# Performance work log

Hardware: AMD Instinct MI355X
Metric: run time of the kernel (lower is better)

## Reference

```python
import jax, jax.numpy as jnp
import numpy as np

N = 100000      # nodes
IN = 256        # in_feats
H = 256         # h_feats
C = 2           # num_classes
E = 400000      # edges per relation
DST_MAX = [70000, 80000, 75000]  # dst ranges -> guarantees isolated nodes per relation


def _build_rel(rng, dst_max):
    """Build one relation: edges, degree mask, induced subgraph on non-isolated nodes."""
    src = rng.integers(0, N, size=E)
    dst = rng.integers(0, dst_max, size=E)
    deg = np.bincount(dst, minlength=N)
    keep = np.where(deg > 0)[0].astype(np.int32)   # nodes with in_degree > 0 (original order)
    iso = np.where(deg == 0)[0].astype(np.int32)   # isolated nodes (original order)
    inv = np.full(N, -1, dtype=np.int64)
    inv[keep] = np.arange(len(keep))
    m = inv[src] >= 0                              # DGL node subgraph keeps edges with both endpoints in set
    ssrc = inv[src[m]].astype(np.int32)
    sdst = inv[dst[m]].astype(np.int32)
    sdeg = np.bincount(sdst, minlength=len(keep))
    norm = (1.0 / np.sqrt(np.clip(sdeg, 1, None))).astype(np.float32)  # D^{-1/2}, clamp(min=1)
    return keep, iso, ssrc, sdst, norm


def setup_inputs() -> dict:
    rng = np.random.default_rng(0)
    key = jax.random.key(0)
    ks = jax.random.split(key, 20)
    d = {"in_feat": jax.random.normal(ks[0], (N, IN), jnp.float32)}
    for r, dm in enumerate(DST_MAX):
        keep, iso, ssrc, sdst, norm = _build_rel(rng, dm)
        d[f"keep{r}"] = jnp.asarray(keep)
        d[f"iso{r}"] = jnp.asarray(iso)
        d[f"src{r}"] = jnp.asarray(ssrc)
        d[f"dst{r}"] = jnp.asarray(sdst)
        d[f"norm{r}"] = jnp.asarray(norm)
        d[f"lam{r}"] = jnp.float32(1.99)  # stand-in for dgl.laplacian_lambda_max (~2 for large graphs)
    s = 0.02
    def W(k, i, o):
        return s * jax.random.normal(k, (i, o), jnp.float32)
    d["W_lin"] = W(ks[1], IN, H);   d["b_lin"] = jnp.zeros((H,), jnp.float32)
    d["W2"]    = W(ks[2], H, H);    d["b2"]    = jnp.zeros((H,), jnp.float32)
    d["W1sg"]  = W(ks[3], H, H);    d["b1sg"]  = jnp.zeros((H,), jnp.float32)
    d["W2sg"]  = W(ks[4], H, H);    d["b2sg"]  = jnp.zeros((H,), jnp.float32)
    d["Wc1"]   = W(ks[5], 2 * H, H); d["bc1"]  = jnp.zeros((H,), jnp.float32)  # ChebConv k=2: Linear(k*H, H)
    d["Wc2"]   = W(ks[6], 2 * H, H); d["bc2"]  = jnp.zeros((H,), jnp.float32)
    d["W3"]    = W(ks[7], 2 * H, H); d["b3"]   = jnp.zeros((H,), jnp.float32)
    d["W4"]    = W(ks[8], H, C);    d["b4"]    = jnp.zeros((C,), jnp.float32)
    return d


def _cheb(x, src, dst, norm, lam, Wc, bc):
    """DGL ChebConv, k=2: X0=x; X1=-re*(D^-.5 A D^-.5 x)+(re-1)*x; relu(Linear([X0,X1]))."""
    re = 2.0 / lam
    xn = x * norm[:, None]
    agg = jax.ops.segment_sum(xn[src], dst, num_segments=x.shape[0]) * norm[:, None]
    X1 = -re * agg + x * (re - 1.0)
    return jax.nn.relu(jnp.concatenate([x, X1], axis=-1) @ Wc + bc)


def reference(in_feat,
              keep0, iso0, src0, dst0, norm0, lam0,
              keep1, iso1, src1, dst1, norm1, lam1,
              keep2, iso2, src2, dst2, norm2, lam2,
              W_lin, b_lin, W2, b2, W1sg, b1sg, W2sg, b2sg,
              Wc1, bc1, Wc2, bc2, W3, b3, W4, b4):
    def block(h, keep, iso, src, dst, norm, lam):
        hk = h[keep]                                   # non-isolated nodes
        h01 = _cheb(hk, src, dst, norm, lam, Wc1, bc1)
        h11 = _cheb(h01, src, dst, norm, lam, Wc2, bc2)
        h02 = h[iso] @ W1sg + b1sg                     # isolated-node branch
        h12 = h02 @ W2sg + b2sg
        h_final = jnp.concatenate([
            jnp.concatenate([h01, h11], axis=-1),      # [M, 2H]
            jnp.concatenate([h02, h12], axis=-1),      # [N-M, 2H]
        ], axis=0)                                     # note: permuted node order, as in original
        return h_final @ W3 + b3

    h = jax.nn.leaky_relu(in_feat @ W_lin + b_lin)
    h = jax.nn.leaky_relu(h @ W2 + b2)
    h_all = []
    rels = [(keep0, iso0, src0, dst0, norm0, lam0),
            (keep1, iso1, src1, dst1, norm1, lam1),
            (keep2, iso2, src2, dst2, norm2, lam2)]
    for rel in rels:
        h = block(h, *rel)   # h is re-used across relations, faithfully to the torch code
        h_all.append(h)
    out = jax.nn.leaky_relu(h_all[0] + h_all[1] + h_all[2])
    return out @ W4 + b4
```

## Files before the change

kernel.cpp:

```cpp
#include <hip/hip_runtime.h>
#include <cstddef>

typedef unsigned short bf16;
typedef short bf16x8 __attribute__((ext_vector_type(8)));
typedef float f32x4 __attribute__((ext_vector_type(4)));
#define LREL 0.01f

__device__ __forceinline__ float bf2f(unsigned int u) {
    union { unsigned int i; float f; } c; c.i = u << 16; return c.f;
}
__device__ __forceinline__ bf16 f2bf(float f) {
    union { unsigned int i; float f; } c; c.f = f;
    return (bf16)((c.i + 0x7FFFu + ((c.i >> 16) & 1u)) >> 16);
}
__device__ __forceinline__ unsigned int pack2(float a, float b) {
    return (unsigned int)f2bf(a) | ((unsigned int)f2bf(b) << 16);
}
__device__ __forceinline__ float activate(float v, int ACT) {
    if (ACT == 1) return v > 0.f ? v : 0.f;
    if (ACT == 2) return v > 0.f ? v : LREL * v;
    return v;
}

template<int ACT, bool DUAL, int ACCMODE, bool GATHER, bool AFP32>
__global__ __launch_bounds__(256) void gemm_mfma(
    const void* __restrict__ A1v, const int* __restrict__ rows1,
    const bf16* __restrict__ A2,
    const bf16* __restrict__ WT1, const bf16* __restrict__ WT2,
    const float* __restrict__ bias,
    bf16* __restrict__ C, bf16* __restrict__ Cacc, int M)
{
    __shared__ bf16 As[128 * 64];
    __shared__ bf16 Bs[128 * 64];
    const int tid  = threadIdx.x;
    const int lane = tid & 63;
    const int wv   = tid >> 6;
    const int wr   = wv >> 1, wc = wv & 1;
    const int row0 = blockIdx.y * 128;
    const int col0 = blockIdx.x * 128;

    f32x4 acc[4][4];
#pragma unroll
    for (int mi = 0; mi < 4; ++mi)
#pragma unroll
        for (int ni = 0; ni < 4; ++ni)
#pragma unroll
            for (int e = 0; e < 4; ++e) acc[mi][ni][e] = 0.f;

    const int ar = tid & 127;
    const int kh = tid >> 7;
    const int arow = min(row0 + ar, M - 1);
    const size_t aoff1 = (size_t)(GATHER ? rows1[arow] : arow) * 256;
    const size_t aoff2 = (size_t)arow * 256;
    const int bn = ar;

    const int nparts = DUAL ? 2 : 1;
    for (int part = 0; part < nparts; ++part) {
        const bf16* __restrict__ WT = (part == 0) ? WT1 : WT2;
        for (int kt = 0; kt < 256; kt += 64) {
            uint4 areg[4], breg[4];
#pragma unroll
            for (int cc = 0; cc < 4; ++cc) {
                const int c = kh * 4 + cc;
                if (part == 0) {
                    if constexpr (AFP32) {
                        const float* p = (const float*)A1v + aoff1 + kt + c * 8;
                        float4 f0 = *(const float4*)p;
                        float4 f1 = *(const float4*)(p + 4);
                        areg[cc].x = pack2(f0.x, f0.y); areg[cc].y = pack2(f0.z, f0.w);
                        areg[cc].z = pack2(f1.x, f1.y); areg[cc].w = pack2(f1.z, f1.w);
                    } else {
                        areg[cc] = *(const uint4*)((const bf16*)A1v + aoff1 + kt + c * 8);
                    }
                } else {
                    areg[cc] = *(const uint4*)(A2 + aoff2 + kt + c * 8);
                }
                breg[cc] = *(const uint4*)(WT + (size_t)(col0 + bn) * 256 + kt + c * 8);
            }
            __syncthreads();
#pragma unroll
            for (int cc = 0; cc < 4; ++cc) {
                const int c = kh * 4 + cc;
                *(uint4*)(As + ar * 64 + 8 * (c ^ (ar & 7))) = areg[cc];
                *(uint4*)(Bs + bn * 64 + 8 * (c ^ (bn & 7))) = breg[cc];
            }
            __syncthreads();
#pragma unroll
            for (int ks = 0; ks < 2; ++ks) {
                bf16x8 af[4], bfr[4];
#pragma unroll
                for (int mi = 0; mi < 4; ++mi) {
                    const int r = wr * 64 + mi * 16 + (lane & 15);
                    const int c = ks * 4 + (lane >> 4);
                    af[mi] = *(const bf16x8*)(As + r * 64 + 8 * (c ^ (r & 7)));
                }
#pragma unroll
                for (int ni = 0; ni < 4; ++ni) {
                    const int n = wc * 64 + ni * 16 + (lane & 15);
                    const int c = ks * 4 + (lane >> 4);
                    bfr[ni] = *(const bf16x8*)(Bs + n * 64 + 8 * (c ^ (n & 7)));
                }
#pragma unroll
                for (int mi = 0; mi < 4; ++mi)
#pragma unroll
                    for (int ni = 0; ni < 4; ++ni)
                        acc[mi][ni] = __builtin_amdgcn_mfma_f32_16x16x32_bf16(
                            bfr[ni], af[mi], acc[mi][ni], 0, 0, 0);
            }
        }
    }

#pragma unroll
    for (int mi = 0; mi < 4; ++mi) {
        const int r = row0 + wr * 64 + mi * 16 + (lane & 15);
        if (r < M) {
#pragma unroll
            for (int ni = 0; ni < 4; ++ni) {
                const int c0 = col0 + wc * 64 + ni * 16 + (lane >> 4) * 4;
                float o[4];
#pragma unroll
                for (int reg = 0; reg < 4; ++reg)
                    o[reg] = activate(acc[mi][ni][reg] + bias[c0 + reg], ACT);
                uint2 cv; cv.x = pack2(o[0], o[1]); cv.y = pack2(o[2], o[3]);
                *(uint2*)(C + (size_t)r * 256 + c0) = cv;
                if constexpr (ACCMODE == 1) {
                    *(uint2*)(Cacc + (size_t)r * 256 + c0) = cv;
                } else if constexpr (ACCMODE == 2) {
                    uint2 ov = *(const uint2*)(Cacc + (size_t)r * 256 + c0);
                    uint2 nv2;
                    nv2.x = pack2(bf2f(ov.x & 0xFFFFu) + o[0], bf2f(ov.x >> 16) + o[1]);
                    nv2.y = pack2(bf2f(ov.y & 0xFFFFu) + o[2], bf2f(ov.y >> 16) + o[3]);
                    *(uint2*)(Cacc + (size_t)r * 256 + c0) = nv2;
                }
            }
        }
    }
}

__global__ void wconv_all(const float* __restrict__ W_lin, const float* __restrict__ W2,
                          const float* __restrict__ W1sg, const float* __restrict__ W2sg,
                          const float* __restrict__ Wc1, const float* __restrict__ Wc2,
                          const float* __restrict__ W3, bf16* __restrict__ out)
{
    const int b = blockIdx.x;
    const int m = b >> 8, k = b & 255, n = threadIdx.x;
    const float* src;
    switch (m) {
        case 0: src = W_lin; break;       case 1: src = W2; break;
        case 2: src = W1sg; break;        case 3: src = W2sg; break;
        case 4: src = Wc1; break;         case 5: src = Wc1 + 65536; break;
        case 6: src = Wc2; break;         case 7: src = Wc2 + 65536; break;
        case 8: src = W3; break;          default: src = W3 + 65536; break;
    }
    out[(size_t)m * 65536 + n * 256 + k] = f2bf(src[k * 256 + n]);
}

template<bool GATHER>
__global__ void agg_x1(const bf16* __restrict__ x, const int* __restrict__ gidx,
                       const float* __restrict__ norm,
                       const int* __restrict__ rp, const int* __restrict__ ssrc,
                       const float* __restrict__ lam, bf16* __restrict__ X1, int M)
{
    int d = blockIdx.x * 4 + (threadIdx.x >> 6);
    if (d >= M) return;
    int l = threadIdx.x & 63;
    float s0 = 0.f, s1 = 0.f, s2 = 0.f, s3 = 0.f;
    int e0 = rp[d], e1 = rp[d + 1];
    for (int e = e0; e < e1; ++e) {
        int si = ssrc[e];
        float nv = norm[si];
        const bf16* xr = x + (size_t)(GATHER ? gidx[si] : si) * 256 + l * 4;
        uint2 u = *(const uint2*)xr;
        s0 += bf2f(u.x & 0xFFFFu) * nv; s1 += bf2f(u.x >> 16) * nv;
        s2 += bf2f(u.y & 0xFFFFu) * nv; s3 += bf2f(u.y >> 16) * nv;
    }
    float re = 2.0f / lam[0];
    float a = -re * norm[d];
    float b = re - 1.0f;
    const bf16* xdp = x + (size_t)(GATHER ? gidx[d] : d) * 256 + l * 4;
    uint2 xd = *(const uint2*)xdp;
    uint2 o;
    o.x = pack2(a * s0 + b * bf2f(xd.x & 0xFFFFu), a * s1 + b * bf2f(xd.x >> 16));
    o.y = pack2(a * s2 + b * bf2f(xd.y & 0xFFFFu), a * s3 + b * bf2f(xd.y >> 16));
    *(uint2*)(X1 + (size_t)d * 256 + l * 4) = o;
}

__global__ void zero_k(int* __restrict__ p, int n)
{
    int i = blockIdx.x * 256 + threadIdx.x;
    if (i < n) p[i] = 0;
}

__global__ void hist_k(const int* __restrict__ dst, int* __restrict__ deg, int E)
{
    int e = blockIdx.x * 256 + threadIdx.x;
    if (e < E) atomicAdd(&deg[dst[e]], 1);
}

__global__ void scan1_k(const int* __restrict__ deg, int* __restrict__ bsum, int M)
{
    __shared__ int red[256];
    int b = blockIdx.x, t = threadIdx.x;
    int base = b * 1024 + t * 4;
    int s = 0;
#pragma unroll
    for (int j = 0; j < 4; ++j) { int i = base + j; if (i < M) s += deg[i]; }
    red[t] = s; __syncthreads();
    for (int off = 128; off; off >>= 1) {
        if (t < off) red[t] += red[t + off];
        __syncthreads();
    }
    if (t == 0) bsum[b] = red[0];
}
__global__ void scan2_k(int* __restrict__ bsum, int nb, int* __restrict__ rp, int M)
{
    __shared__ int buf[256];
    int t = threadIdx.x;
    int v = (t < nb) ? bsum[t] : 0;
    buf[t] = v; __syncthreads();
    for (int off = 1; off < 256; off <<= 1) {
        int y = (t >= off) ? buf[t - off] : 0;
        __syncthreads();
        buf[t] += y;
        __syncthreads();
    }
    if (t < nb) bsum[t] = buf[t] - v;
    if (t == 0) rp[M] = buf[255];
}
__global__ void scan3_k(const int* __restrict__ deg, const int* __restrict__ bsum,
                        int* __restrict__ rp, int M)
{
    __shared__ int buf[256];
    int b = blockIdx.x, t = threadIdx.x;
    int base = b * 1024 + t * 4;
    int v0 = (base + 0 < M) ? deg[base + 0] : 0;
    int v1 = (base + 1 < M) ? deg[base + 1] : 0;
    int v2 = (base + 2 < M) ? deg[base + 2] : 0;
    int v3 = (base + 3 < M) ? deg[base + 3] : 0;
    int s = v0 + v1 + v2 + v3;
    buf[t] = s; __syncthreads();
    for (int off = 1; off < 256; off <<= 1) {
        int y = (t >= off) ? buf[t - off] : 0;
        __syncthreads();
        buf[t] += y;
        __syncthreads();
    }
    int ex = bsum[b] + buf[t] - s;
    if (base + 0 < M) rp[base + 0] = ex;
    if (base + 1 < M) rp[base + 1] = ex + v0;
    if (base + 2 < M) rp[base + 2] = ex + v0 + v1;
    if (base + 3 < M) rp[base + 3] = ex + v0 + v1 + v2;
}

__global__ void scatter_k(const int* __restrict__ src, const int* __restrict__ dst,
                          const int* __restrict__ rp, int* __restrict__ cursor,
                          int* __restrict__ out, int E)
{
    int e = blockIdx.x * 256 + threadIdx.x;
    if (e < E) {
        int d = dst[e];
        int pos = rp[d] + atomicAdd(&cursor[d], 1);
        out[pos] = src[e];
    }
}

__global__ void final_k(const bf16* __restrict__ acc, const float* __restrict__ W4,
                        const float* __restrict__ b4, float* __restrict__ out, int Nn)
{
    int r = blockIdx.x * 4 + (threadIdx.x >> 6);
    if (r >= Nn) return;
    int l = threadIdx.x & 63;
    uint2 u = *(const uint2*)(acc + (size_t)r * 256 + l * 4);
    float v[4] = { bf2f(u.x & 0xFFFFu), bf2f(u.x >> 16),
                   bf2f(u.y & 0xFFFFu), bf2f(u.y >> 16) };
    float s0 = 0.f, s1 = 0.f;
#pragma unroll
    for (int j = 0; j < 4; ++j) {
        float x = v[j] > 0.f ? v[j] : LREL * v[j];
        int k = l * 4 + j;
        s0 += x * W4[k * 2 + 0];
        s1 += x * W4[k * 2 + 1];
    }
#pragma unroll
    for (int off = 32; off; off >>= 1) {
        s0 += __shfl_xor(s0, off, 64);
        s1 += __shfl_xor(s1, off, 64);
    }
    if (l == 0) {
        out[(size_t)r * 2 + 0] = s0 + b4[0];
        out[(size_t)r * 2 + 1] = s1 + b4[1];
    }
}

extern "C" void kernel_launch(void* const* d_in, const int* in_sizes, int n_in,
                              void* d_out, int out_size, void* d_ws, size_t ws_size,
                              hipStream_t stream)
{
    const float* in_feat = (const float*)d_in[0];
    const int Nn = in_sizes[0] / 256;

    const float* W_lin = (const float*)d_in[19]; const float* b_lin = (const float*)d_in[20];
    const float* W2p   = (const float*)d_in[21]; const float* b2   = (const float*)d_in[22];
    const float* W1sg  = (const float*)d_in[23]; const float* b1sg = (const float*)d_in[24];
    const float* W2sg  = (const float*)d_in[25]; const float* b2sg = (const float*)d_in[26];
    const float* Wc1   = (const float*)d_in[27]; const float* bc1  = (const float*)d_in[28];
    const float* Wc2   = (const float*)d_in[29]; const float* bc2  = (const float*)d_in[30];
    const float* W3p   = (const float*)d_in[31]; const float* b3   = (const float*)d_in[32];
    const float* W4p   = (const float*)d_in[33]; const float* b4   = (const float*)d_in[34];

    int Mr[3], NIr[3], Er[3];
    int M_max = 0, NI_max = 0, E_max = 0;
    for (int r = 0; r < 3; ++r) {
        Mr[r]  = in_sizes[1 + 6 * r];
        NIr[r] = in_sizes[2 + 6 * r];
        Er[r]  = in_sizes[3 + 6 * r];
        if (Mr[r] > M_max)  M_max  = Mr[r];
        if (NIr[r] > NI_max) NI_max = NIr[r];
        if (Er[r] > E_max)  E_max  = Er[r];
    }

    bf16* ACC = (bf16*)d_ws;
    bf16* H   = ACC + (size_t)Nn * 256;
    bf16* S1  = H + (size_t)Nn * 256;
    bf16* S2  = S1 + (size_t)M_max * 256;
    bf16* S3  = S2 + (size_t)M_max * 256;
    bf16* S4  = S3 + (size_t)M_max * 256;
    bf16* WTb = S4 + (size_t)NI_max * 256;
    int* deg    = (int*)(WTb + 10 * 65536);
    int* cursor = deg + (Nn + 1);
    int* rp     = cursor + (Nn + 1);
    int* bsum   = rp + (Nn + 1);
    int* ssrc   = bsum + 256;

    bf16* WT_lin = WTb;             bf16* WT_2   = WTb + 1 * 65536;
    bf16* WT_1sg = WTb + 2 * 65536; bf16* WT_2sg = WTb + 3 * 65536;
    bf16* WT_c1a = WTb + 4 * 65536; bf16* WT_c1b = WTb + 5 * 65536;
    bf16* WT_c2a = WTb + 6 * 65536; bf16* WT_c2b = WTb + 7 * 65536;
    bf16* WT_3a  = WTb + 8 * 65536; bf16* WT_3b  = WTb + 9 * 65536;

    auto g2 = [](int M) { return dim3(2u, (unsigned)((M + 127) / 128)); };

    wconv_all<<<2560, 256, 0, stream>>>(W_lin, W2p, W1sg, W2sg, Wc1, Wc2, W3p, WTb);

    gemm_mfma<2, false, 0, false, true><<<g2(Nn), 256, 0, stream>>>(
        in_feat, nullptr, nullptr, WT_lin, nullptr, b_lin, ACC, nullptr, Nn);
    gemm_mfma<2, false, 0, false, false><<<g2(Nn), 256, 0, stream>>>(
        ACC, nullptr, nullptr, WT_2, nullptr, b2, H, nullptr, Nn);

    for (int r = 0; r < 3; ++r) {
        const int*   keep = (const int*)d_in[1 + 6 * r];
        const int*   iso  = (const int*)d_in[2 + 6 * r];
        const int*   srcA = (const int*)d_in[3 + 6 * r];
        const int*   dstA = (const int*)d_in[4 + 6 * r];
        const float* norm = (const float*)d_in[5 + 6 * r];
        const float* lam  = (const float*)d_in[6 + 6 * r];
        const int M  = Mr[r];
        const int NI = NIr[r];
        const int E  = Er[r];
        const int nb = (M + 1023) / 1024;

        zero_k<<<(2 * (Nn + 1) + 255) / 256, 256, 0, stream>>>(deg, 2 * (Nn + 1));
        hist_k<<<(E + 255) / 256, 256, 0, stream>>>(dstA, deg, E);
        scan1_k<<<nb, 256, 0, stream>>>(deg, bsum, M);
        scan2_k<<<1, 256, 0, stream>>>(bsum, nb, rp, M);
        scan3_k<<<nb, 256, 0, stream>>>(deg, bsum, rp, M);
        scatter_k<<<(E + 255) / 256, 256, 0, stream>>>(srcA, dstA, rp, cursor, ssrc, E);

        agg_x1<true><<<(M + 3) / 4, 256, 0, stream>>>(H, keep, norm, rp, ssrc, lam, S1, M);
        gemm_mfma<1, true, 0, true, false><<<g2(M), 256, 0, stream>>>(
            H, keep, S1, WT_c1a, WT_c1b, bc1, S2, nullptr, M);
        agg_x1<false><<<(M + 3) / 4, 256, 0, stream>>>(S2, nullptr, norm, rp, ssrc, lam, S1, M);
        gemm_mfma<1, true, 0, false, false><<<g2(M), 256, 0, stream>>>(
            S2, nullptr, S1, WT_c2a, WT_c2b, bc2, S3, nullptr, M);

        gemm_mfma<0, false, 0, true, false><<<g2(NI), 256, 0, stream>>>(
            H, iso, nullptr, WT_1sg, nullptr, b1sg, S1, nullptr, NI);
        gemm_mfma<0, false, 0, false, false><<<g2(NI), 256, 0, stream>>>(
            S1, nullptr, nullptr, WT_2sg, nullptr, b2sg, S4, nullptr, NI);

        if (r == 0) {
            gemm_mfma<0, true, 1, false, false><<<g2(NI), 256, 0, stream>>>(
                S1, nullptr, S4, WT_3a, WT_3b, b3,
                H + (size_t)M * 256, ACC + (size_t)M * 256, NI);
            gemm_mfma<0, true, 1, false, false><<<g2(M), 256, 0, stream>>>(
                S2, nullptr, S3, WT_3a, WT_3b, b3, H, ACC, M);
        } else {
            gemm_mfma<0, true, 2, false, false><<<g2(NI), 256, 0, stream>>>(
                S1, nullptr, S4, WT_3a, WT_3b, b3,
                H + (size_t)M * 256, ACC + (size_t)M * 256, NI);
            gemm_mfma<0, true, 2, false, false><<<g2(M), 256, 0, stream>>>(
                S2, nullptr, S3, WT_3a, WT_3b, b3, H, ACC, M);
        }
    }

    final_k<<<(Nn + 3) / 4, 256, 0, stream>>>(ACC, W4p, b4, (float*)d_out, Nn);
}
```

Baseline: 2.576 ms.

## Widen GEMM tile to full 256 output columns so A rows load once

The MFMA GEMM now uses 128x256 tiles. Each block covers all 256 output columns and each wave owns a 64-column slice across all 128 rows. Before, the grid split the columns in two, so every A row (including gathered and fp32-converted rows) was fetched and converted twice; now it is fetched once per block. The cost is doubled B shared memory (48KB total LDS), twice the accumulators per thread (128 floats), half as many blocks, and possibly lower occupancy.

After: 2.476 ms. 1.04x faster.

```diff
diff --git a/kernel.cpp b/kernel.cpp
--- a/kernel.cpp
+++ b/kernel.cpp
@@ -31,37 +31,34 @@
     bf16* __restrict__ C, bf16* __restrict__ Cacc, int M)
 {
     __shared__ bf16 As[128 * 64];
-    __shared__ bf16 Bs[128 * 64];
+    __shared__ bf16 Bs[256 * 64];
     const int tid  = threadIdx.x;
     const int lane = tid & 63;
     const int wv   = tid >> 6;
-    const int wr   = wv >> 1, wc = wv & 1;
-    const int row0 = blockIdx.y * 128;
-    const int col0 = blockIdx.x * 128;
-
-    f32x4 acc[4][4];
-#pragma unroll
-    for (int mi = 0; mi < 4; ++mi)
+    const int row0 = blockIdx.x * 128;
+
+    f32x4 acc[8][4];
+#pragma unroll
+    for (int mi = 0; mi < 8; ++mi)
 #pragma unroll
         for (int ni = 0; ni < 4; ++ni)
 #pragma unroll
             for (int e = 0; e < 4; ++e) acc[mi][ni][e] = 0.f;
 
     const int ar = tid & 127;
-    const int kh = tid >> 7;
+    const int ah = tid >> 7;
     const int arow = min(row0 + ar, M - 1);
     const size_t aoff1 = (size_t)(GATHER ? rows1[arow] : arow) * 256;
     const size_t aoff2 = (size_t)arow * 256;
-    const int bn = ar;
 
     const int nparts = DUAL ? 2 : 1;
     for (int part = 0; part < nparts; ++part) {
         const bf16* __restrict__ WT = (part == 0) ? WT1 : WT2;
         for (int kt = 0; kt < 256; kt += 64) {
-            uint4 areg[4], breg[4];
+            uint4 areg[4], breg[8];
 #pragma unroll
             for (int cc = 0; cc < 4; ++cc) {
-                const int c = kh * 4 + cc;
+                const int c = ah * 4 + cc;
                 if (part == 0) {
                     if constexpr (AFP32) {
                         const float* p = (const float*)A1v + aoff1 + kt + c * 8;
@@ -75,48 +72,49 @@
                 } else {
                     areg[cc] = *(const uint4*)(A2 + aoff2 + kt + c * 8);
                 }
-                breg[cc] = *(const uint4*)(WT + (size_t)(col0 + bn) * 256 + kt + c * 8);
             }
+#pragma unroll
+            for (int cc = 0; cc < 8; ++cc)
+                breg[cc] = *(const uint4*)(WT + (size_t)tid * 256 + kt + cc * 8);
             __syncthreads();
 #pragma unroll
             for (int cc = 0; cc < 4; ++cc) {
-                const int c = kh * 4 + cc;
+                const int c = ah * 4 + cc;
                 *(uint4*)(As + ar * 64 + 8 * (c ^ (ar & 7))) = areg[cc];
-                *(uint4*)(Bs + bn * 64 + 8 * (c ^ (bn & 7))) = breg[cc];
             }
+#pragma unroll
+            for (int cc = 0; cc < 8; ++cc)
+                *(uint4*)(Bs + tid * 64 + 8 * (cc ^ (tid & 7))) = breg[cc];
             __syncthreads();
 #pragma unroll
             for (int ks = 0; ks < 2; ++ks) {
-                bf16x8 af[4], bfr[4];
-#pragma unroll
-                for (int mi = 0; mi < 4; ++mi) {
-                    const int r = wr * 64 + mi * 16 + (lane & 15);
-                    const int c = ks * 4 + (lane >> 4);
-                    af[mi] = *(const bf16x8*)(As + r * 64 + 8 * (c ^ (r & 7)));
-                }
+                const int c = ks * 4 + (lane >> 4);
+                bf16x8 bfr[4];
 #pragma unroll
                 for (int ni = 0; ni < 4; ++ni) {
-                    const int n = wc * 64 + ni * 16 + (lane & 15);
-                    const int c = ks * 4 + (lane >> 4);
+                    const int n = wv * 64 + ni * 16 + (lane & 15);
                     bfr[ni] = *(const bf16x8*)(Bs + n * 64 + 8 * (c ^ (n & 7)));
                 }
 #pragma unroll
-                for (int mi = 0; mi < 4; ++mi)
+                for (int mi = 0; mi < 8; ++mi) {
+                    const int r = mi * 16 + (lane & 15);
+                    bf16x8 af = *(const bf16x8*)(As + r * 64 + 8 * (c ^ (r & 7)));
 #pragma unroll
                     for (int ni = 0; ni < 4; ++ni)
                         acc[mi][ni] = __builtin_amdgcn_mfma_f32_16x16x32_bf16(
-                            bfr[ni], af[mi], acc[mi][ni], 0, 0, 0);
+                            bfr[ni], af, acc[mi][ni], 0, 0, 0);
+                }
             }
         }
     }
 
 #pragma unroll
-    for (int mi = 0; mi < 4; ++mi) {
-        const int r = row0 + wr * 64 + mi * 16 + (lane & 15);
+    for (int mi = 0; mi < 8; ++mi) {
+        const int r = row0 + mi * 16 + (lane & 15);
         if (r < M) {
 #pragma unroll
             for (int ni = 0; ni < 4; ++ni) {
-                const int c0 = col0 + wc * 64 + ni * 16 + (lane >> 4) * 4;
+                const int c0 = wv * 64 + ni * 16 + (lane >> 4) * 4;
                 float o[4];
 #pragma unroll
                 for (int reg = 0; reg < 4; ++reg)
@@ -338,13 +336,13 @@
     bf16* WT_c2a = WTb + 6 * 65536; bf16* WT_c2b = WTb + 7 * 65536;
     bf16* WT_3a  = WTb + 8 * 65536; bf16* WT_3b  = WTb + 9 * 65536;
 
-    auto g2 = [](int M) { return dim3(2u, (unsigned)((M + 127) / 128)); };
+    auto g1 = [](int M) { return dim3((unsigned)((M + 127) / 128)); };
 
     wconv_all<<<2560, 256, 0, stream>>>(W_lin, W2p, W1sg, W2sg, Wc1, Wc2, W3p, WTb);
 
-    gemm_mfma<2, false, 0, false, true><<<g2(Nn), 256, 0, stream>>>(
+    gemm_mfma<2, false, 0, false, true><<<g1(Nn), 256, 0, stream>>>(
         in_feat, nullptr, nullptr, WT_lin, nullptr, b_lin, ACC, nullptr, Nn);
-    gemm_mfma<2, false, 0, false, false><<<g2(Nn), 256, 0, stream>>>(
+    gemm_mfma<2, false, 0, false, false><<<g1(Nn), 256, 0, stream>>>(
         ACC, nullptr, nullptr, WT_2, nullptr, b2, H, nullptr, Nn);
 
     for (int r = 0; r < 3; ++r) {
@@ -367,28 +365,28 @@
         scatter_k<<<(E + 255) / 256, 256, 0, stream>>>(srcA, dstA, rp, cursor, ssrc, E);
 
         agg_x1<true><<<(M + 3) / 4, 256, 0, stream>>>(H, keep, norm, rp, ssrc, lam, S1, M);
-        gemm_mfma<1, true, 0, true, false><<<g2(M), 256, 0, stream>>>(
+        gemm_mfma<1, true, 0, true, false><<<g1(M), 256, 0, stream>>>(
             H, keep, S1, WT_c1a, WT_c1b, bc1, S2, nullptr, M);
         agg_x1<false><<<(M + 3) / 4, 256, 0, stream>>>(S2, nullptr, norm, rp, ssrc, lam, S1, M);
-        gemm_mfma<1, true, 0, false, false><<<g2(M), 256, 0, stream>>>(
+        gemm_mfma<1, true, 0, false, false><<<g1(M), 256, 0, stream>>>(
             S2, nullptr, S1, WT_c2a, WT_c2b, bc2, S3, nullptr, M);
 
-        gemm_mfma<0, false, 0, true, false><<<g2(NI), 256, 0, stream>>>(
+        gemm_mfma<0, false, 0, true, false><<<g1(NI), 256, 0, stream>>>(
             H, iso, nullptr, WT_1sg, nullptr, b1sg, S1, nullptr, NI);
-        gemm_mfma<0, false, 0, false, false><<<g2(NI), 256, 0, stream>>>(
+        gemm_mfma<0, false, 0, false, false><<<g1(NI), 256, 0, stream>>>(
             S1, nullptr, nullptr, WT_2sg, nullptr, b2sg, S4, nullptr, NI);
 
         if (r == 0) {
-            gemm_mfma<0, true, 1, false, false><<<g2(NI), 256, 0, stream>>>(
+            gemm_mfma<0, true, 1, false, false><<<g1(NI), 256, 0, stream>>>(
                 S1, nullptr, S4, WT_3a, WT_3b, b3,
                 H + (size_t)M * 256, ACC + (size_t)M * 256, NI);
-            gemm_mfma<0, true, 1, false, false><<<g2(M), 256, 0, stream>>>(
+            gemm_mfma<0, true, 1, false, false><<<g1(M), 256, 0, stream>>>(
                 S2, nullptr, S3, WT_3a, WT_3b, b3, H, ACC, M);
         } else {
-            gemm_mfma<0, true, 2, false, false><<<g2(NI), 256, 0, stream>>>(
+            gemm_mfma<0, true, 2, false, false><<<g1(NI), 256, 0, stream>>>(
                 S1, nullptr, S4, WT_3a, WT_3b, b3,
                 H + (size_t)M * 256, ACC + (size_t)M * 256, NI);
-            gemm_mfma<0, true, 2, false, false><<<g2(M), 256, 0, stream>>>(
+            gemm_mfma<0, true, 2, false, false><<<g1(M), 256, 0, stream>>>(
                 S2, nullptr, S3, WT_3a, WT_3b, b3, H, ACC, M);
         }
     }
```
